# Kernel tuning notes

Hardware: AMD Instinct MI355X
Metric: run time of the kernel (lower is better)

The kernel has to match this reference:

```python
import jax, jax.numpy as jnp
import numpy as np

N, H, V = 8192, 1024, 32000
IGNORE_INDEX = -100
LABEL_SMOOTHING = 0.0
LOGIT_SCALE = 1.0


def setup_inputs() -> dict:
    key = jax.random.key(0)
    k1, k2, k3 = jax.random.split(key, 3)
    x = jax.random.normal(k1, (N, H), dtype=jnp.float32)
    weight = jax.random.normal(k2, (V, H), dtype=jnp.float32) * 0.02
    bias = jnp.zeros((V,), dtype=jnp.float32)
    target = jax.random.randint(k3, (N,), 0, V, dtype=jnp.int64)
    return {"x": x, "weight": weight, "bias": bias, "target": target}


def reference(x, weight, bias, target):
    # logits: [N, V]; fused kernel never materializes this fully, but math is identical
    logits = (x @ weight.T + bias) * LOGIT_SCALE
    lse = jax.nn.logsumexp(logits.astype(jnp.float32), axis=-1)  # [N]
    valid = target != IGNORE_INDEX
    safe_t = jnp.where(valid, target, 0)
    tgt_logit = jnp.take_along_axis(logits, safe_t[:, None], axis=-1)[:, 0]
    loss_i = lse - tgt_logit
    if LABEL_SMOOTHING > 0:
        eps = LABEL_SMOOTHING / V
        z = (-eps * logits).sum(-1)
        loss_i = loss_i * (1.0 - LABEL_SMOOTHING) + (z + LABEL_SMOOTHING * lse)
    loss_i = jnp.where(valid, loss_i, 0.0)
    total = jnp.maximum(valid.sum(), 1)
    # reduction == 'mean': each per-token loss divided by total, then summed
    return loss_i.sum() / total
```

## Files before the change

### kernel.cpp

```cpp
#include <hip/hip_runtime.h>
#include <math.h>

typedef int    intx8    __attribute__((ext_vector_type(8)));
typedef float  floatx16 __attribute__((ext_vector_type(16)));

#define N_ROWS 8192
#define H_DIM  1024
#define V_DIM  32000
#define V_PAD  32768
#define IGNORE_INDEX (-100)

#define S_SPLITS 16
#define TILES_PER_SPLIT 16
#define BM 256
#define BN 128
#define BK 64
#define KSTEPS 16
#define TOTAL_STEPS (TILES_PER_SPLIT * KSTEPS)

#define LOG2E 1.4426950408889634f
#define LN2   0.6931471805599453f

__global__ __launch_bounds__(256) void convert_fp8(const float* __restrict__ in,
                                                   unsigned char* __restrict__ out,
                                                   int Rstride, float scale) {
  const int r = blockIdx.x * 256 + threadIdx.x;
  const int u = blockIdx.y;
  const float4* src = (const float4*)(in + (size_t)r * H_DIM + u * 16);
  uint4 res;
#pragma unroll
  for (int j = 0; j < 4; ++j) {
    const float4 v = src[j];
    int p = __builtin_amdgcn_cvt_pk_fp8_f32(v.x * scale, v.y * scale, 0, false);
    p = __builtin_amdgcn_cvt_pk_fp8_f32(v.z * scale, v.w * scale, p, true);
    ((int*)&res)[j] = p;
  }
  *(uint4*)(out + ((size_t)u * Rstride + r) * 16) = res;
}

__global__ __launch_bounds__(256) void pad_bias(const float* __restrict__ bias,
                                                float* __restrict__ biasp) {
  const int i = blockIdx.x * 256 + threadIdx.x;
  biasp[i] = (i < V_DIM) ? bias[i] * LOG2E : -1e30f;
}


#define STAGE(ST, CUR) do {                                                              \
    const int _ss = (ST);                                                                \
    const int _ks = _ss & 15;                                                            \
    const int _ct = _ss >> 4;                                                            \
    const int _ub = _ks * 4;                                                             \
    const int _n0 = (sidx * TILES_PER_SPLIT + _ct) * BN;                                 \
    _Pragma("unroll")                                                                    \
    for (int _j = 0; _j < 4; ++_j) {                                                     \
      const int _c = _j * 4 + w, _u = _c >> 2, _rb = _c & 3;                             \
      __builtin_amdgcn_global_load_lds(                                                  \
          (const __attribute__((address_space(1))) void*)(xs +                           \
              ((size_t)(_ub + _u) * N_ROWS + row0 + _rb * 64 + lane) * 16),              \
          (__attribute__((address_space(3))) void*)(smA + (CUR) * (4 * 256 * 16) +       \
              (_u * 256 + _rb * 64 + lane) * 16),                                        \
          16, 0, 0);                                                                     \
    }                                                                                    \
    _Pragma("unroll")                                                                    \
    for (int _j = 0; _j < 2; ++_j) {                                                     \
      const int _c = _j * 4 + w, _u = _c >> 1, _rb = _c & 1;                             \
      __builtin_amdgcn_global_load_lds(                                                  \
          (const __attribute__((address_space(1))) void*)(wsb +                          \
              ((size_t)(_ub + _u) * V_PAD + _n0 + _rb * 64 + lane) * 16),                \
          (__attribute__((address_space(3))) void*)(smB + (CUR) * (4 * 128 * 16) +       \
              (_u * 128 + _rb * 64 + lane) * 16),                                        \
          16, 0, 0);                                                                     \
    }                                                                                    \
  } while (0)

#define DO_STEP(ST, CUR) do {                                                            \
    const int _st = (ST);                                                                \
                     \
    if (_st < TOTAL_STEPS - 1) asm volatile("s_waitcnt vmcnt(6)" ::: "memory");          \
    else                       asm volatile("s_waitcnt vmcnt(0)" ::: "memory");          \
    __builtin_amdgcn_sched_barrier(0);                                                   \
    __builtin_amdgcn_s_barrier();                     \
    union { intx8 v; uint4 q[2]; } a[2], b[4];                                           \
    {                                                                                    \
      const int ua = half * 2;                                                           \
      _Pragma("unroll")                                                                  \
      for (int mb = 0; mb < 2; ++mb) {                                                   \
        a[mb].q[0] = *(const uint4*)(smA + (CUR) * (4 * 256 * 16) +                      \
                                     ((ua * 256 + wr + mb * 32 + l31) * 16));            \
        a[mb].q[1] = *(const uint4*)(smA + (CUR) * (4 * 256 * 16) +                      \
                                     (((ua + 1) * 256 + wr + mb * 32 + l31) * 16));      \
      }                                                                                  \
      _Pragma("unroll")                                                                  \
      for (int nb = 0; nb < 4; ++nb) {                                                   \
        b[nb].q[0] = *(const uint4*)(smB + (CUR) * (4 * 128 * 16) +                      \
                                     ((ua * 128 + nb * 32 + l31) * 16));                 \
        b[nb].q[1] = *(const uint4*)(smB + (CUR) * (4 * 128 * 16) +                      \
                                     (((ua + 1) * 128 + nb * 32 + l31) * 16));           \
      }                                                                                  \
    }                                                                                    \
    asm volatile("s_waitcnt lgkmcnt(0)" ::: "memory");        \
    __builtin_amdgcn_sched_barrier(0);                                                   \
    __builtin_amdgcn_s_barrier();                   \
    __builtin_amdgcn_sched_barrier(0);                                                   \
    if (_st + 2 < TOTAL_STEPS) STAGE(_st + 2, CUR);           \
    __builtin_amdgcn_sched_barrier(0);                                                   \
    __builtin_amdgcn_s_setprio(1);                                                       \
    _Pragma("unroll")                                                                    \
    for (int mb = 0; mb < 2; ++mb)                                                       \
      _Pragma("unroll")                                                                  \
      for (int nb = 0; nb < 4; ++nb)                                                     \
        acc[mb][nb] = __builtin_amdgcn_mfma_scale_f32_32x32x64_f8f6f4(                   \
            a[mb].v, b[nb].v, acc[mb][nb],                                               \
            0, 0,                                                  \
            0, 0x7F7F7F7F,                                            \
            0, 0x7F7F7F7F);                                           \
    __builtin_amdgcn_s_setprio(0);                                                       \
  } while (0)

__global__ __launch_bounds__(256, 2) void flce_main(const unsigned char* __restrict__ xs,
                                                    const unsigned char* __restrict__ wsb,
                                                    const float* __restrict__ biasp,
                                                    float* __restrict__ partials) {
  __shared__ __align__(16) unsigned char smA[2 * 4 * 256 * 16];
  __shared__ __align__(16) unsigned char smB[2 * 4 * 128 * 16];
  __shared__ __align__(16) float sbias[TILES_PER_SPLIT * BN];

  const int tid  = threadIdx.x;
  const int lane = tid & 63;
  const int w    = tid >> 6;
  const int l31  = lane & 31;
  const int half = lane >> 5;
  const int wr   = w * 64;
  const int row0 = blockIdx.x * BM;
  const int sidx = blockIdx.y;

  float l_state[32];
#pragma unroll
  for (int i = 0; i < 32; ++i) l_state[i] = 0.f;

#pragma unroll
  for (int j = 0; j < 2; ++j) {
    const int c = j * 4 + w;
    __builtin_amdgcn_global_load_lds(
        (const __attribute__((address_space(1))) void*)(biasp +
            (size_t)sidx * (TILES_PER_SPLIT * BN) + c * 256 + lane * 4),
        (__attribute__((address_space(3))) void*)(sbias + c * 256 + lane * 4),
        16, 0, 0);
  }
  STAGE(0, 0);
  STAGE(1, 1);

#pragma unroll 1
  for (int ct = 0; ct < TILES_PER_SPLIT; ++ct) {
    floatx16 acc[2][4];
#pragma unroll
    for (int mb = 0; mb < 2; ++mb)
#pragma unroll
      for (int nb = 0; nb < 4; ++nb)
#pragma unroll
        for (int i = 0; i < 16; ++i) acc[mb][nb][i] = 0.f;

#pragma unroll 1
    for (int ks2 = 0; ks2 < 8; ++ks2) {
      const int st0 = ct * 16 + ks2 * 2;
      DO_STEP(st0, 0);
      DO_STEP(st0 + 1, 1);
    }

    float bnb[4];
#pragma unroll
    for (int nb = 0; nb < 4; ++nb) bnb[nb] = sbias[ct * BN + nb * 32 + l31];
#pragma unroll
    for (int mb = 0; mb < 2; ++mb)
#pragma unroll
      for (int r = 0; r < 16; ++r) {
        float s = exp2f(acc[mb][0][r] + bnb[0]) + exp2f(acc[mb][1][r] + bnb[1])
                + exp2f(acc[mb][2][r] + bnb[2]) + exp2f(acc[mb][3][r] + bnb[3]);
        l_state[mb * 16 + r] += s;
      }
  }

#pragma unroll
  for (int s = 0; s < 32; ++s) {
    float v = l_state[s];
#pragma unroll
    for (int off = 1; off < 32; off <<= 1) v += __shfl_xor(v, off, 64);
    l_state[s] = v;
  }

  if (l31 == 0) {
#pragma unroll
    for (int s = 0; s < 32; ++s) {
      const int mb = s >> 4, r = s & 15;
      const int row = wr + mb * 32 + 4 * half + (r & 3) + 8 * (r >> 2);
      partials[(size_t)(row0 + row) * S_SPLITS + sidx] = l_state[s];
    }
  }
}

__global__ __launch_bounds__(256) void tgt_kernel(const float* __restrict__ x,
                                                  const float* __restrict__ wgt,
                                                  const float* __restrict__ bias,
                                                  const int* __restrict__ target,
                                                  float* __restrict__ tgt_logit) {
  const int r = blockIdx.x * 4 + (threadIdx.x >> 6);
  const int lane = threadIdx.x & 63;
  const int t = target[r];
  const int tt = (t == IGNORE_INDEX) ? 0 : t;
  const float4* xr = (const float4*)(x + (size_t)r * H_DIM);
  const float4* wr = (const float4*)(wgt + (size_t)tt * H_DIM);
  float acc = 0.f;
#pragma unroll
  for (int i = 0; i < 4; ++i) {
    const float4 a = xr[lane + i * 64];
    const float4 b = wr[lane + i * 64];
    acc += a.x * b.x + a.y * b.y + a.z * b.z + a.w * b.w;
  }
#pragma unroll
  for (int off = 32; off >= 1; off >>= 1) acc += __shfl_xor(acc, off, 64);
  if (lane == 0) tgt_logit[r] = acc + bias[tt];
}

__global__ __launch_bounds__(256) void loss_rows(const float* __restrict__ partials,
                                                 const float* __restrict__ tgt_logit,
                                                 const int* __restrict__ target,
                                                 float* __restrict__ bsums) {
  const int r = blockIdx.x * 256 + threadIdx.x;
  float l = 0.f;
#pragma unroll
  for (int s = 0; s < S_SPLITS; ++s) l += partials[(size_t)r * S_SPLITS + s];
  const float lse = LN2 * __log2f(l);
  const bool valid = (target[r] != IGNORE_INDEX);
  float loss = valid ? (lse - tgt_logit[r]) : 0.f;
  float cnt  = valid ? 1.f : 0.f;
  const int lane = threadIdx.x & 63;
  const int w = threadIdx.x >> 6;
#pragma unroll
  for (int off = 32; off >= 1; off >>= 1) {
    loss += __shfl_xor(loss, off, 64);
    cnt  += __shfl_xor(cnt, off, 64);
  }
  __shared__ float sl[4], sc[4];
  if (lane == 0) { sl[w] = loss; sc[w] = cnt; }
  __syncthreads();
  if (threadIdx.x == 0) {
    float S = 0.f, C = 0.f;
    for (int i = 0; i < 4; ++i) { S += sl[i]; C += sc[i]; }
    bsums[blockIdx.x] = S;
    bsums[32 + blockIdx.x] = C;
  }
}

__global__ void finalize(const float* __restrict__ bsums, float* __restrict__ out) {
  const int t = threadIdx.x;
  float s = (t < 32) ? bsums[t] : 0.f;
  float c = (t < 32) ? bsums[32 + t] : 0.f;
#pragma unroll
  for (int off = 32; off >= 1; off >>= 1) {
    s += __shfl_xor(s, off, 64);
    c += __shfl_xor(c, off, 64);
  }
  if (t == 0) out[0] = s / fmaxf(c, 1.f);
}

extern "C" void kernel_launch(void* const* d_in, const int* in_sizes, int n_in,
                              void* d_out, int out_size, void* d_ws, size_t ws_size,
                              hipStream_t stream) {
  const float* x    = (const float*)d_in[0];
  const float* wgt  = (const float*)d_in[1];
  const float* bias = (const float*)d_in[2];
  const int*   tgt  = (const int*)d_in[3];
  float* out = (float*)d_out;

  char* ws = (char*)d_ws;
  const size_t XS8 = (size_t)N_ROWS * H_DIM;
  const size_t WS8 = (size_t)V_PAD * H_DIM;
  const size_t BP  = (size_t)V_PAD * 4;
  const size_t PB  = (size_t)N_ROWS * S_SPLITS * 4;
  unsigned char* xs8 = (unsigned char*)ws;
  unsigned char* ws8 = (unsigned char*)(ws + XS8);
  float* biasp    = (float*)(ws + XS8 + WS8);
  float* partials = (float*)(ws + XS8 + WS8 + BP);
  float* tgt_lg   = (float*)(ws + XS8 + WS8 + BP + PB);
  float* bsums    = (float*)(ws + XS8 + WS8 + BP + PB + (size_t)N_ROWS * 4);

  convert_fp8<<<dim3(N_ROWS / 256, H_DIM / 16), 256, 0, stream>>>(x, xs8, N_ROWS, LOG2E);
  convert_fp8<<<dim3(V_DIM / 256, H_DIM / 16), 256, 0, stream>>>(wgt, ws8, V_PAD, 1.0f);
  pad_bias<<<V_PAD / 256, 256, 0, stream>>>(bias, biasp);
  tgt_kernel<<<N_ROWS / 4, 256, 0, stream>>>(x, wgt, bias, tgt, tgt_lg);
  flce_main<<<dim3(N_ROWS / BM, S_SPLITS), 256, 0, stream>>>(xs8, ws8, biasp, partials);
  loss_rows<<<N_ROWS / 256, 256, 0, stream>>>(partials, tgt_lg, tgt, bsums);
  finalize<<<1, 64, 0, stream>>>(bsums, out);
}
```

Before: 548.1 us.

## Load A fragments directly into registers, drop LDS staging for A and bias

The activation (A) tile is no longer staged through LDS. Each wave loads its own FP8 A fragments straight from global memory into registers, double-buffered across steps, while only the weight tile keeps going through LDS via async global-to-LDS DMA. The prefetch distance drops from two steps to one, the explicit vmcnt/lgkmcnt waits are replaced by a single __syncthreads per step, and bias is read from global memory instead of LDS. Block indices are also remapped so that neighbouring workgroups share row blocks and splits, which should improve L2 reuse. The change cuts LDS footprint and traffic but adds register pressure and exposes global load latency with a shallower pipeline.

```diff
diff --git a/kernel.cpp b/kernel.cpp
--- a/kernel.cpp
+++ b/kernel.cpp
@@ -14,9 +14,9 @@
 #define TILES_PER_SPLIT 16
 #define BM 256
 #define BN 128
-#define BK 64
 #define KSTEPS 16
 #define TOTAL_STEPS (TILES_PER_SPLIT * KSTEPS)
+#define BBUF (4 * 128 * 16)
 
 #define LOG2E 1.4426950408889634f
 #define LN2   0.6931471805599453f
@@ -45,72 +45,54 @@
 }
 
 
-#define STAGE(ST, CUR) do {                                                              \
-    const int _ss = (ST);                                                                \
-    const int _ks = _ss & 15;                                                            \
-    const int _ct = _ss >> 4;                                                            \
-    const int _ub = _ks * 4;                                                             \
-    const int _n0 = (sidx * TILES_PER_SPLIT + _ct) * BN;                                 \
-    _Pragma("unroll")                                                                    \
-    for (int _j = 0; _j < 4; ++_j) {                                                     \
-      const int _c = _j * 4 + w, _u = _c >> 2, _rb = _c & 3;                             \
-      __builtin_amdgcn_global_load_lds(                                                  \
-          (const __attribute__((address_space(1))) void*)(xs +                           \
-              ((size_t)(_ub + _u) * N_ROWS + row0 + _rb * 64 + lane) * 16),              \
-          (__attribute__((address_space(3))) void*)(smA + (CUR) * (4 * 256 * 16) +       \
-              (_u * 256 + _rb * 64 + lane) * 16),                                        \
-          16, 0, 0);                                                                     \
-    }                                                                                    \
+typedef union { intx8 v; uint4 q[2]; } afrag;
+
+#define BDMA(T) do {                                                                     \
+    const int _t = (T);                                                                  \
+    const int _ub = (_t & 15) * 4;                                                       \
+    const int _n0 = (sidx * TILES_PER_SPLIT + (_t >> 4)) * BN;                           \
+    unsigned char* _d = smB + ((_t & 1) ? BBUF : 0);                                     \
     _Pragma("unroll")                                                                    \
     for (int _j = 0; _j < 2; ++_j) {                                                     \
       const int _c = _j * 4 + w, _u = _c >> 1, _rb = _c & 1;                             \
       __builtin_amdgcn_global_load_lds(                                                  \
           (const __attribute__((address_space(1))) void*)(wsb +                          \
               ((size_t)(_ub + _u) * V_PAD + _n0 + _rb * 64 + lane) * 16),                \
-          (__attribute__((address_space(3))) void*)(smB + (CUR) * (4 * 128 * 16) +       \
-              (_u * 128 + _rb * 64 + lane) * 16),                                        \
+          (__attribute__((address_space(3))) void*)(_d + ((_u * 128 + _rb * 64 + lane) * 16)), \
           16, 0, 0);                                                                     \
     }                                                                                    \
   } while (0)
 
-#define DO_STEP(ST, CUR) do {                                                            \
-    const int _st = (ST);                                                                \
-                     \
-    if (_st < TOTAL_STEPS - 1) asm volatile("s_waitcnt vmcnt(6)" ::: "memory");          \
-    else                       asm volatile("s_waitcnt vmcnt(0)" ::: "memory");          \
-    __builtin_amdgcn_sched_barrier(0);                                                   \
-    __builtin_amdgcn_s_barrier();                     \
-    union { intx8 v; uint4 q[2]; } a[2], b[4];                                           \
-    {                                                                                    \
-      const int ua = half * 2;                                                           \
-      _Pragma("unroll")                                                                  \
-      for (int mb = 0; mb < 2; ++mb) {                                                   \
-        a[mb].q[0] = *(const uint4*)(smA + (CUR) * (4 * 256 * 16) +                      \
-                                     ((ua * 256 + wr + mb * 32 + l31) * 16));            \
-        a[mb].q[1] = *(const uint4*)(smA + (CUR) * (4 * 256 * 16) +                      \
-                                     (((ua + 1) * 256 + wr + mb * 32 + l31) * 16));      \
-      }                                                                                  \
-      _Pragma("unroll")                                                                  \
-      for (int nb = 0; nb < 4; ++nb) {                                                   \
-        b[nb].q[0] = *(const uint4*)(smB + (CUR) * (4 * 128 * 16) +                      \
-                                     ((ua * 128 + nb * 32 + l31) * 16));                 \
-        b[nb].q[1] = *(const uint4*)(smB + (CUR) * (4 * 128 * 16) +                      \
-                                     (((ua + 1) * 128 + nb * 32 + l31) * 16));           \
-      }                                                                                  \
+#define ALD(T, DST) do {                                                                 \
+    const int _u2 = ((T) & 15) * 4 + half * 2;                                           \
+    DST[0].q[0] = *(const uint4*)(xs + (((size_t)(_u2    ) * N_ROWS + arow0) * 16));     \
+    DST[0].q[1] = *(const uint4*)(xs + (((size_t)(_u2 + 1) * N_ROWS + arow0) * 16));     \
+    DST[1].q[0] = *(const uint4*)(xs + (((size_t)(_u2    ) * N_ROWS + arow1) * 16));     \
+    DST[1].q[1] = *(const uint4*)(xs + (((size_t)(_u2 + 1) * N_ROWS + arow1) * 16));     \
+  } while (0)
+
+#define STEP(T, AU, AL) do {                                                             \
+    const int _st = (T);                                                                 \
+    __syncthreads();       \
+    if (_st + 1 < TOTAL_STEPS) {                                                         \
+      BDMA(_st + 1);                                                                     \
+      ALD(_st + 1, AL);                                                                  \
     }                                                                                    \
-    asm volatile("s_waitcnt lgkmcnt(0)" ::: "memory");        \
-    __builtin_amdgcn_sched_barrier(0);                                                   \
-    __builtin_amdgcn_s_barrier();                   \
-    __builtin_amdgcn_sched_barrier(0);                                                   \
-    if (_st + 2 < TOTAL_STEPS) STAGE(_st + 2, CUR);           \
-    __builtin_amdgcn_sched_barrier(0);                                                   \
+    const unsigned char* _pB = smB + ((_st & 1) ? BBUF : 0);                             \
+    afrag b[4];                                                                          \
+    const int _ua = half * 2;                                                            \
+    _Pragma("unroll")                                                                    \
+    for (int nb = 0; nb < 4; ++nb) {                                                     \
+      b[nb].q[0] = *(const uint4*)(_pB + ((_ua * 128 + nb * 32 + l31) * 16));            \
+      b[nb].q[1] = *(const uint4*)(_pB + (((_ua + 1) * 128 + nb * 32 + l31) * 16));      \
+    }                                                                                    \
     __builtin_amdgcn_s_setprio(1);                                                       \
     _Pragma("unroll")                                                                    \
     for (int mb = 0; mb < 2; ++mb)                                                       \
       _Pragma("unroll")                                                                  \
       for (int nb = 0; nb < 4; ++nb)                                                     \
         acc[mb][nb] = __builtin_amdgcn_mfma_scale_f32_32x32x64_f8f6f4(                   \
-            a[mb].v, b[nb].v, acc[mb][nb],                                               \
+            AU[mb].v, b[nb].v, acc[mb][nb],                                              \
             0, 0,                                                  \
             0, 0x7F7F7F7F,                                            \
             0, 0x7F7F7F7F);                                           \
@@ -121,9 +103,7 @@
                                                     const unsigned char* __restrict__ wsb,
                                                     const float* __restrict__ biasp,
                                                     float* __restrict__ partials) {
-  __shared__ __align__(16) unsigned char smA[2 * 4 * 256 * 16];
-  __shared__ __align__(16) unsigned char smB[2 * 4 * 128 * 16];
-  __shared__ __align__(16) float sbias[TILES_PER_SPLIT * BN];
+  __shared__ __align__(16) unsigned char smB[2 * BBUF];
 
   const int tid  = threadIdx.x;
   const int lane = tid & 63;
@@ -131,24 +111,23 @@
   const int l31  = lane & 31;
   const int half = lane >> 5;
   const int wr   = w * 64;
-  const int row0 = blockIdx.x * BM;
-  const int sidx = blockIdx.y;
+
+  const int hw     = blockIdx.y * 32 + blockIdx.x;
+  const int rowblk = hw >> 4;
+  const int sidx   = ((hw & 7) << 1) | ((hw >> 3) & 1);
+  const int row0   = rowblk * BM;
+
+  const size_t arow0 = (size_t)(row0 + wr + l31);
+  const size_t arow1 = arow0 + 32;
 
   float l_state[32];
 #pragma unroll
   for (int i = 0; i < 32; ++i) l_state[i] = 0.f;
 
-#pragma unroll
-  for (int j = 0; j < 2; ++j) {
-    const int c = j * 4 + w;
-    __builtin_amdgcn_global_load_lds(
-        (const __attribute__((address_space(1))) void*)(biasp +
-            (size_t)sidx * (TILES_PER_SPLIT * BN) + c * 256 + lane * 4),
-        (__attribute__((address_space(3))) void*)(sbias + c * 256 + lane * 4),
-        16, 0, 0);
-  }
-  STAGE(0, 0);
-  STAGE(1, 1);
+  afrag aE[2], aO[2];
+
+  BDMA(0);
+  ALD(0, aE);
 
 #pragma unroll 1
   for (int ct = 0; ct < TILES_PER_SPLIT; ++ct) {
@@ -162,14 +141,15 @@
 
 #pragma unroll 1
     for (int ks2 = 0; ks2 < 8; ++ks2) {
-      const int st0 = ct * 16 + ks2 * 2;
-      DO_STEP(st0, 0);
-      DO_STEP(st0 + 1, 1);
+      const int st0 = ct * KSTEPS + ks2 * 2;
+      STEP(st0,     aE, aO);
+      STEP(st0 + 1, aO, aE);
     }
 
+    const int n0 = (sidx * TILES_PER_SPLIT + ct) * BN;
     float bnb[4];
 #pragma unroll
-    for (int nb = 0; nb < 4; ++nb) bnb[nb] = sbias[ct * BN + nb * 32 + l31];
+    for (int nb = 0; nb < 4; ++nb) bnb[nb] = biasp[n0 + nb * 32 + l31];
 #pragma unroll
     for (int mb = 0; mb < 2; ++mb)
 #pragma unroll
```

After: 555.0 us. About the same (+1.3%).
